# Kernel optimization log

Hardware: AMD Instinct MI355X
Metric: run time of the kernel (lower is better)

Reference implementation:

```python
import jax, jax.numpy as jnp
import numpy as np

N = 2048      # num_nodes
B = 16        # batch
D_IN = 2      # input_dim per node
UNITS = 64    # rnn_units
F = D_IN + UNITS   # concat feature size = 66
M = 3         # num_matrices = (1 support + 1 adp hop)*K(=1) + 1 identity
E = N * 16    # sparse support edges (avg degree 16)


def _spmm(rows, cols, vals, x):
    # sparse support @ x, x: (N, K); equivalent of torch.sparse.mm
    return jax.ops.segment_sum(vals[:, None] * x[cols], rows, num_segments=N)


def _gconv(inputs, state, W, support_rows, support_cols, support_vals, adp):
    # inputs: (B, N*D_IN), state: (B, N*units) -> out: (B, N*out_dim)
    x = jnp.concatenate([inputs.reshape(B, N, -1), state.reshape(B, N, -1)], axis=2)  # (B,N,F)
    f = x.shape[2]
    x0 = x.transpose(1, 2, 0).reshape(N, f * B)                # (N, F*B)
    # diffusion step 1 over the single random_walk support
    x1 = _spmm(support_rows, support_cols, support_vals, x0)   # (N, F*B)
    # adaptive adjacency, k_hop=1 -> adp_lst = [adp], applied to x0
    x_temp = x0.reshape(N, f, B).transpose(2, 0, 1)            # (B,N,F)
    x2 = jnp.einsum('bnm,bmf->bnf', adp, x_temp)               # (B,N,F)
    x2 = x2.transpose(1, 2, 0).reshape(N, f * B)
    xs = jnp.stack([x0, x1, x2], axis=0)                       # (M,N,F*B)
    xs = xs.reshape(M, N, f, B).transpose(3, 1, 2, 0).reshape(B * N, f * M)
    out = xs @ W                                               # (B*N, out_dim)  (no bias: source never adds it)
    return out.reshape(B, N * W.shape[1])


def setup_inputs() -> dict:
    key = jax.random.key(0)
    ks = jax.random.split(key, 8)
    inputs = jax.random.normal(ks[0], (B, N * D_IN), dtype=jnp.float32)
    hx = jax.random.normal(ks[1], (B, N * UNITS), dtype=jnp.float32)
    adp = jax.random.uniform(ks[2], (B, N, N), dtype=jnp.float32) / N  # ~row-stochastic adaptive adj
    support_rows = jax.random.randint(ks[3], (E,), 0, N, dtype=jnp.int32)
    support_cols = jax.random.randint(ks[4], (E,), 0, N, dtype=jnp.int32)
    support_vals = jax.random.uniform(ks[5], (E,), dtype=jnp.float32) / 16.0
    W_ru = jax.random.normal(ks[6], (F * M, 2 * UNITS), dtype=jnp.float32) * 0.05
    W_c = jax.random.normal(ks[7], (F * M, UNITS), dtype=jnp.float32) * 0.05
    return dict(inputs=inputs, hx=hx, adp=adp, support_rows=support_rows,
                support_cols=support_cols, support_vals=support_vals,
                W_ru=W_ru, W_c=W_c, time_axis=0)


def reference(inputs, hx, adp, support_rows, support_cols, support_vals, W_ru, W_c, time_axis):
    # GRU with graph convolution gates (use_gc_for_ru=True, activation=tanh)
    ru = jax.nn.sigmoid(_gconv(inputs, hx, W_ru, support_rows, support_cols, support_vals, adp))
    ru = ru.reshape(B, N, 2 * UNITS)
    r = ru[..., :UNITS].reshape(B, N * UNITS)
    u = ru[..., UNITS:].reshape(B, N * UNITS)
    c = jnp.tanh(_gconv(inputs, r * hx, W_c, support_rows, support_cols, support_vals, adp))
    return u * hx + (1.0 - u) * c
```

## Files before the change

### kernel.cpp

```cpp
#include <hip/hip_runtime.h>
#include <cstdint>
#include <cstddef>

#define DN 2048
#define DB 16
#define DE 32768
#define FPAD 96

typedef __bf16 bf16x8 __attribute__((ext_vector_type(8)));
typedef float f32x4 __attribute__((ext_vector_type(4)));

__global__ __launch_bounds__(256) void prep_kernel(
    const float* __restrict__ inputs, const float* __restrict__ hx,
    const float* __restrict__ Wru, const float* __restrict__ Wc,
    __bf16* __restrict__ xcat1, __bf16* __restrict__ xcat2,
    __bf16* __restrict__ wtru, __bf16* __restrict__ wtc,
    int* __restrict__ cnt) {
  int idx = blockIdx.x * 256 + threadIdx.x;
  const int T1 = DB * DN * FPAD;
  if (idx < 2 * T1) {
    int which = idx >= T1 ? 1 : 0;
    int i = idx - which * T1;
    int f = i % FPAD;
    int bn = i / FPAD;
    int n = bn & (DN - 1);
    int b = bn >> 11;
    __bf16 v = (__bf16)0.0f;
    if (f < 2) v = (__bf16)inputs[(b << 12) + n * 2 + f];
    else if (f < 66 && !which) v = (__bf16)hx[((size_t)b << 17) + (n << 6) + (f - 2)];
    if (which) xcat2[i] = v; else xcat1[i] = v;
  } else {
    int j = idx - 2 * T1;
    if (j < 384 * FPAD) {
      int k = j % FPAD, o = j / FPAD;
      wtru[j] = (k < 66) ? (__bf16)Wru[(k * 3 + (o >> 7)) * 128 + (o & 127)] : (__bf16)0.0f;
    } else {
      j -= 384 * FPAD;
      if (j < 192 * FPAD) {
        int k = j % FPAD, o = j / FPAD;
        wtc[j] = (k < 66) ? (__bf16)Wc[(k * 3 + (o >> 6)) * 64 + (o & 63)] : (__bf16)0.0f;
      } else {
        j -= 192 * FPAD;
        if (j < DN) cnt[j] = 0;
      }
    }
  }
}

__global__ __launch_bounds__(512) void csr_count(const int* __restrict__ rows,
                                                 int* __restrict__ cnt) {
  int e = blockIdx.x * 512 + threadIdx.x;
  atomicAdd(&cnt[rows[e]], 1);
}

__global__ __launch_bounds__(1024) void csr_scan(const int* __restrict__ cnt,
                                                 int* __restrict__ csr_ptr,
                                                 int* __restrict__ off) {
  __shared__ int sa[DN];
  __shared__ int sb[DN];
  int t = threadIdx.x;
  int c0 = cnt[t], c1 = cnt[t + 1024];
  sa[t] = c0; sa[t + 1024] = c1;
  __syncthreads();
  int* src = sa; int* dst = sb;
  for (int o = 1; o < DN; o <<= 1) {
    for (int i = t; i < DN; i += 1024) {
      int v = src[i];
      if (i >= o) v += src[i - o];
      dst[i] = v;
    }
    __syncthreads();
    int* tmp = src; src = dst; dst = tmp;
  }
  int e0 = src[t] - c0;
  int e1 = src[t + 1024] - c1;
  csr_ptr[t] = e0; csr_ptr[t + 1024] = e1;
  off[t] = e0; off[t + 1024] = e1;
  if (t == 0) csr_ptr[DN] = DE;
}

__global__ __launch_bounds__(512) void csr_scatter(
    const int* __restrict__ rows, const int* __restrict__ cols,
    const float* __restrict__ vals, int* __restrict__ off,
    int* __restrict__ csr_col, float* __restrict__ csr_val) {
  int e = blockIdx.x * 512 + threadIdx.x;
  int r = rows[e];
  int p = atomicAdd(&off[r], 1);
  csr_col[p] = cols[e];
  csr_val[p] = vals[e];
}

template <int OD>
__global__ __launch_bounds__(256) void small_gemm(
    const __bf16* __restrict__ A, const __bf16* __restrict__ Bt,
    float* __restrict__ Y0, __bf16* __restrict__ y1b, __bf16* __restrict__ y2b) {
  __shared__ __attribute__((aligned(16))) __bf16 As[128 * 104];
  __shared__ __attribute__((aligned(16))) __bf16 Bs[64 * 104];
  int tid = threadIdx.x;
  int wave = tid >> 6, lane = tid & 63;
  int lrow = lane & 15, quad = lane >> 4;
  int r0 = blockIdx.x * 128;
  int c0 = blockIdx.y * 64;
  const uint4* gA = (const uint4*)(A + (size_t)r0 * FPAD);
  const uint4* gB = (const uint4*)(Bt + (size_t)c0 * FPAD);
  uint4* sA = (uint4*)As;
  uint4* sB = (uint4*)Bs;
#pragma unroll
  for (int i = 0; i < 6; ++i) {
    int s = i * 256 + tid;
    int r = s / 12, c4 = s % 12;
    sA[r * 13 + c4] = gA[r * 12 + c4];
  }
#pragma unroll
  for (int i = 0; i < 3; ++i) {
    int s = i * 256 + tid;
    int r = s / 12, c4 = s % 12;
    sB[r * 13 + c4] = gB[r * 12 + c4];
  }
  __syncthreads();
  int wm = wave >> 1, wn = wave & 1;
  f32x4 acc[4][2];
#pragma unroll
  for (int mt = 0; mt < 4; ++mt)
#pragma unroll
    for (int nt = 0; nt < 2; ++nt) acc[mt][nt] = (f32x4){0.f, 0.f, 0.f, 0.f};
#pragma unroll
  for (int kk = 0; kk < 3; ++kk) {
    bf16x8 af[4], bv[2];
#pragma unroll
    for (int mt = 0; mt < 4; ++mt)
      af[mt] = *(const bf16x8*)(As + (wm * 64 + mt * 16 + lrow) * 104 + kk * 32 + quad * 8);
#pragma unroll
    for (int nt = 0; nt < 2; ++nt)
      bv[nt] = *(const bf16x8*)(Bs + (wn * 32 + nt * 16 + lrow) * 104 + kk * 32 + quad * 8);
#pragma unroll
    for (int mt = 0; mt < 4; ++mt)
#pragma unroll
      for (int nt = 0; nt < 2; ++nt)
        acc[mt][nt] = __builtin_amdgcn_mfma_f32_16x16x32_bf16(af[mt], bv[nt], acc[mt][nt], 0, 0, 0);
  }
#pragma unroll
  for (int mt = 0; mt < 4; ++mt)
#pragma unroll
    for (int nt = 0; nt < 2; ++nt)
#pragma unroll
      for (int r = 0; r < 4; ++r) {
        int row = r0 + wm * 64 + mt * 16 + quad * 4 + r;
        int col = c0 + wn * 32 + nt * 16 + lrow;
        float v = acc[mt][nt][r];
        int g = col >> ((OD == 128) ? 7 : 6);
        int oo = col & (OD - 1);
        size_t oi = (size_t)row * OD + oo;
        if (g == 0) Y0[oi] = v;
        else if (g == 1) y1b[oi] = (__bf16)v;
        else y2b[oi] = (__bf16)v;
      }
}

template <int OD>
__global__ __launch_bounds__(256) void gather_pre(
    float* __restrict__ Y0, const __bf16* __restrict__ y1b,
    const int* __restrict__ csr_ptr, const int* __restrict__ csr_col,
    const float* __restrict__ csr_val) {
  constexpr int SH = (OD == 128) ? 7 : 6;
  int idx = blockIdx.x * 256 + threadIdx.x;
  int o = idx & (OD - 1);
  int bn = idx >> SH;
  int n = bn & (DN - 1);
  int b = bn >> 11;
  float acc = Y0[idx];
  int e1 = csr_ptr[n + 1];
  const __bf16* yb = y1b + ((size_t)b << 11) * OD;
  for (int e = csr_ptr[n]; e < e1; ++e)
    acc += csr_val[e] * (float)yb[(size_t)csr_col[e] * OD + o];
  Y0[idx] = acc;
}

template <int OD>
__global__ void transpose_y2(const __bf16* __restrict__ y2b, __bf16* __restrict__ y2t) {
  __shared__ __bf16 tile[32][33];
  int b = blockIdx.z;
  int mb = blockIdx.x * 32, ob = blockIdx.y * 32;
  int tx = threadIdx.x, ty = threadIdx.y;
#pragma unroll
  for (int i = 0; i < 4; ++i)
    tile[ty + i * 8][tx] = y2b[(size_t)(b * DN + mb + ty + i * 8) * OD + ob + tx];
  __syncthreads();
#pragma unroll
  for (int i = 0; i < 4; ++i)
    y2t[(size_t)(b * OD + ob + ty + i * 8) * DN + mb + tx] = tile[tx][ty + i * 8];
}

template <int OD, bool IS_RU>
__global__ __launch_bounds__(256, 4) void adp_gemm(
    const float* __restrict__ adp, const __bf16* __restrict__ y2t,
    const float* __restrict__ pre, const float* __restrict__ hx,
    float* __restrict__ u_buf, __bf16* __restrict__ xcat2,
    float* __restrict__ outp) {
  constexpr int NT = OD / 32;
  int tid = threadIdx.x;
  int wave = tid >> 6, lane = tid & 63;
  int lrow = lane & 15, quad = lane >> 4;
  int hw = blockIdx.x;
  int swz = (hw & 7) * 128 + (hw >> 3);
  int b = swz >> 6;
  int row0 = (swz & 63) * 32;
  int wm = wave >> 1, wn = wave & 1;
  int arow = row0 + wm * 16 + lrow;
  const float* Ap = adp + ((size_t)b * DN + arow) * DN + quad * 8;
  const __bf16* Bb = y2t + (size_t)b * OD * (size_t)DN + quad * 8;
  const __bf16* Bp[NT];
#pragma unroll
  for (int nt = 0; nt < NT; ++nt)
    Bp[nt] = Bb + (size_t)(wn * (NT * 16) + nt * 16 + lrow) * DN;

  f32x4 acc[NT];
#pragma unroll
  for (int nt = 0; nt < NT; ++nt) acc[nt] = (f32x4){0.f, 0.f, 0.f, 0.f};

  f32x4 aE0, aE1, aE2, aE3, aO0, aO1, aO2, aO3;
#define LOADA(c, a0, a1, a2, a3)                 \
  {                                              \
    const float* p_ = Ap + (size_t)(c) * 64;     \
    a0 = *(const f32x4*)p_;                      \
    a1 = *(const f32x4*)(p_ + 4);                \
    a2 = *(const f32x4*)(p_ + 32);               \
    a3 = *(const f32x4*)(p_ + 36);               \
  }

  LOADA(0, aE0, aE1, aE2, aE3);
  LOADA(1, aO0, aO1, aO2, aO3);

#pragma unroll 1
  for (int c = 0; c < DN / 64; c += 2) {
    {
      bf16x8 bv[2][NT];
#pragma unroll
      for (int kk = 0; kk < 2; ++kk)
#pragma unroll
        for (int nt = 0; nt < NT; ++nt)
          bv[kk][nt] = *(const bf16x8*)(Bp[nt] + c * 64 + kk * 32);
      bf16x8 af0, af1;
#pragma unroll
      for (int j = 0; j < 4; ++j) {
        af0[j] = (__bf16)aE0[j]; af0[4 + j] = (__bf16)aE1[j];
        af1[j] = (__bf16)aE2[j]; af1[4 + j] = (__bf16)aE3[j];
      }
      if (c + 2 < DN / 64) LOADA(c + 2, aE0, aE1, aE2, aE3);
#pragma unroll
      for (int nt = 0; nt < NT; ++nt)
        acc[nt] = __builtin_amdgcn_mfma_f32_16x16x32_bf16(af0, bv[0][nt], acc[nt], 0, 0, 0);
#pragma unroll
      for (int nt = 0; nt < NT; ++nt)
        acc[nt] = __builtin_amdgcn_mfma_f32_16x16x32_bf16(af1, bv[1][nt], acc[nt], 0, 0, 0);
    }
    {
      bf16x8 bv[2][NT];
#pragma unroll
      for (int kk = 0; kk < 2; ++kk)
#pragma unroll
        for (int nt = 0; nt < NT; ++nt)
          bv[kk][nt] = *(const bf16x8*)(Bp[nt] + (c + 1) * 64 + kk * 32);
      bf16x8 af0, af1;
#pragma unroll
      for (int j = 0; j < 4; ++j) {
        af0[j] = (__bf16)aO0[j]; af0[4 + j] = (__bf16)aO1[j];
        af1[j] = (__bf16)aO2[j]; af1[4 + j] = (__bf16)aO3[j];
      }
      if (c + 3 < DN / 64) LOADA(c + 3, aO0, aO1, aO2, aO3);
#pragma unroll
      for (int nt = 0; nt < NT; ++nt)
        acc[nt] = __builtin_amdgcn_mfma_f32_16x16x32_bf16(af0, bv[0][nt], acc[nt], 0, 0, 0);
#pragma unroll
      for (int nt = 0; nt < NT; ++nt)
        acc[nt] = __builtin_amdgcn_mfma_f32_16x16x32_bf16(af1, bv[1][nt], acc[nt], 0, 0, 0);
    }
  }
#undef LOADA

#pragma unroll
  for (int nt = 0; nt < NT; ++nt)
#pragma unroll
    for (int r = 0; r < 4; ++r) {
      int n = row0 + wm * 16 + quad * 4 + r;
      int o = wn * (NT * 16) + nt * 16 + lrow;
      float g = acc[nt][r] + pre[((size_t)b * DN + n) * OD + o];
      if (IS_RU) {
        float s = 1.f / (1.f + __expf(-g));
        if (o < 64) {
          float hxv = hx[((size_t)b << 17) + n * 64 + o];
          xcat2[((size_t)b * DN + n) * FPAD + 2 + o] = (__bf16)(s * hxv);
        } else {
          u_buf[((size_t)b * DN + n) * 64 + (o - 64)] = s;
        }
      } else {
        float cval = 1.f - 2.f / (__expf(2.f * g) + 1.f);
        float u = u_buf[((size_t)b * DN + n) * 64 + o];
        float hxv = hx[((size_t)b << 17) + n * 64 + o];
        outp[((size_t)b << 17) + n * 64 + o] = u * hxv + (1.f - u) * cval;
      }
    }
}

extern "C" void kernel_launch(void* const* d_in, const int* in_sizes, int n_in,
                              void* d_out, int out_size, void* d_ws, size_t ws_size,
                              hipStream_t stream) {
  const float* inputs = (const float*)d_in[0];
  const float* hx     = (const float*)d_in[1];
  const float* adp    = (const float*)d_in[2];
  const int* srows    = (const int*)d_in[3];
  const int* scols    = (const int*)d_in[4];
  const float* svals  = (const float*)d_in[5];
  const float* Wru    = (const float*)d_in[6];
  const float* Wc     = (const float*)d_in[7];
  float* outp = (float*)d_out;

  char* w = (char*)d_ws;
  auto carve = [&](size_t bytes) -> char* {
    char* p = w;
    w += (bytes + 255) & ~(size_t)255;
    return p;
  };
  int*    csr_ptr = (int*)   carve((DN + 1) * sizeof(int));
  int*    csr_col = (int*)   carve(DE * sizeof(int));
  float*  csr_val = (float*) carve(DE * sizeof(float));
  int*    cnt     = (int*)   carve(DN * sizeof(int));
  int*    off     = (int*)   carve(DN * sizeof(int));
  __bf16* xcat1   = (__bf16*)carve((size_t)DB * DN * FPAD * 2);
  __bf16* xcat2   = (__bf16*)carve((size_t)DB * DN * FPAD * 2);
  __bf16* wtru    = (__bf16*)carve(384 * FPAD * 2);
  __bf16* wtc     = (__bf16*)carve(192 * FPAD * 2);
  float*  Y0      = (float*) carve((size_t)DB * DN * 128 * 4);
  __bf16* y1b     = (__bf16*)carve((size_t)DB * DN * 128 * 2);
  __bf16* y2b     = (__bf16*)carve((size_t)DB * DN * 128 * 2);
  __bf16* y2t     = (__bf16*)carve((size_t)DB * DN * 128 * 2);
  float*  u_buf   = (float*) carve((size_t)DB * DN * 64 * 4);
  (void)ws_size; (void)in_sizes; (void)n_in; (void)out_size;

  prep_kernel<<<24800, 256, 0, stream>>>(inputs, hx, Wru, Wc, xcat1, xcat2,
                                         wtru, wtc, cnt);
  csr_count<<<64, 512, 0, stream>>>(srows, cnt);
  csr_scan<<<1, 1024, 0, stream>>>(cnt, csr_ptr, off);
  csr_scatter<<<64, 512, 0, stream>>>(srows, scols, svals, off, csr_col, csr_val);

  small_gemm<128><<<dim3(256, 6), 256, 0, stream>>>(xcat1, wtru, Y0, y1b, y2b);
  gather_pre<128><<<16384, 256, 0, stream>>>(Y0, y1b, csr_ptr, csr_col, csr_val);
  transpose_y2<128><<<dim3(64, 4, 16), dim3(32, 8), 0, stream>>>(y2b, y2t);
  adp_gemm<128, true><<<1024, 256, 0, stream>>>(
      adp, y2t, Y0, hx, u_buf, xcat2, outp);

  small_gemm<64><<<dim3(256, 3), 256, 0, stream>>>(xcat2, wtc, Y0, y1b, y2b);
  gather_pre<64><<<8192, 256, 0, stream>>>(Y0, y1b, csr_ptr, csr_col, csr_val);
  transpose_y2<64><<<dim3(64, 2, 16), dim3(32, 8), 0, stream>>>(y2b, y2t);
  adp_gemm<64, false><<<1024, 256, 0, stream>>>(
      adp, y2t, Y0, hx, u_buf, xcat2, outp);
}
```

Baseline: 796.1 us.

## Write y2 in MFMA-fragment packed layout and drop transpose kernels

The small GEMM now writes the adp-path projection directly into a packed layout that matches the B-fragment order of the adp GEMM MFMA, so the separate transpose kernels are removed. The adp GEMM is retiled to 16-row blocks with each wave owning a column slice. It also uses twice as many blocks and a higher occupancy hint, and drops the manual double-buffered A prefetch. This removes two launches and a round trip through memory and makes B loads fully coalesced. The cost is that each adp row tile is now read by fewer columns per block, and the A stream loses its explicit software prefetch.

```diff
diff --git a/kernel.cpp b/kernel.cpp
--- a/kernel.cpp
+++ b/kernel.cpp
@@ -8,6 +8,7 @@
 #define FPAD 96
 
 typedef __bf16 bf16x8 __attribute__((ext_vector_type(8)));
+typedef __bf16 bf16x4 __attribute__((ext_vector_type(4)));
 typedef float f32x4 __attribute__((ext_vector_type(4)));
 
 __global__ __launch_bounds__(256) void prep_kernel(
@@ -93,7 +94,7 @@
 template <int OD>
 __global__ __launch_bounds__(256) void small_gemm(
     const __bf16* __restrict__ A, const __bf16* __restrict__ Bt,
-    float* __restrict__ Y0, __bf16* __restrict__ y1b, __bf16* __restrict__ y2b) {
+    float* __restrict__ Y0, __bf16* __restrict__ y1b, __bf16* __restrict__ y2p) {
   __shared__ __attribute__((aligned(16))) __bf16 As[128 * 104];
   __shared__ __attribute__((aligned(16))) __bf16 Bs[64 * 104];
   int tid = threadIdx.x;
@@ -142,19 +143,31 @@
 #pragma unroll
   for (int mt = 0; mt < 4; ++mt)
 #pragma unroll
-    for (int nt = 0; nt < 2; ++nt)
-#pragma unroll
-      for (int r = 0; r < 4; ++r) {
-        int row = r0 + wm * 64 + mt * 16 + quad * 4 + r;
-        int col = c0 + wn * 32 + nt * 16 + lrow;
-        float v = acc[mt][nt][r];
-        int g = col >> ((OD == 128) ? 7 : 6);
-        int oo = col & (OD - 1);
-        size_t oi = (size_t)row * OD + oo;
-        if (g == 0) Y0[oi] = v;
-        else if (g == 1) y1b[oi] = (__bf16)v;
-        else y2b[oi] = (__bf16)v;
+    for (int nt = 0; nt < 2; ++nt) {
+      int col = c0 + wn * 32 + nt * 16 + lrow;
+      int g = col >> ((OD == 128) ? 7 : 6);
+      int oo = col & (OD - 1);
+      int rowb = r0 + wm * 64 + mt * 16 + quad * 4;
+      if (g == 2) {
+        int bb = rowb >> 11;
+        int n_ = rowb & 2047;
+        bf16x4 v;
+#pragma unroll
+        for (int r = 0; r < 4; ++r) v[r] = (__bf16)acc[mt][nt][r];
+        size_t off = ((((size_t)bb * (OD / 16) + (oo >> 4)) * 64 + (n_ >> 5)) * 4 +
+                      ((n_ >> 3) & 3)) * 128 + (oo & 15) * 8 + (n_ & 7);
+        *(bf16x4*)(y2p + off) = v;
+      } else {
+#pragma unroll
+        for (int r = 0; r < 4; ++r) {
+          int row = rowb + r;
+          float v = acc[mt][nt][r];
+          size_t oi = (size_t)row * OD + oo;
+          if (g == 0) Y0[oi] = v;
+          else y1b[oi] = (__bf16)v;
+        }
       }
+    }
 }
 
 template <int OD>
@@ -176,114 +189,65 @@
   Y0[idx] = acc;
 }
 
-template <int OD>
-__global__ void transpose_y2(const __bf16* __restrict__ y2b, __bf16* __restrict__ y2t) {
-  __shared__ __bf16 tile[32][33];
-  int b = blockIdx.z;
-  int mb = blockIdx.x * 32, ob = blockIdx.y * 32;
-  int tx = threadIdx.x, ty = threadIdx.y;
-#pragma unroll
-  for (int i = 0; i < 4; ++i)
-    tile[ty + i * 8][tx] = y2b[(size_t)(b * DN + mb + ty + i * 8) * OD + ob + tx];
-  __syncthreads();
-#pragma unroll
-  for (int i = 0; i < 4; ++i)
-    y2t[(size_t)(b * OD + ob + ty + i * 8) * DN + mb + tx] = tile[tx][ty + i * 8];
-}
-
 template <int OD, bool IS_RU>
-__global__ __launch_bounds__(256, 4) void adp_gemm(
-    const float* __restrict__ adp, const __bf16* __restrict__ y2t,
+__global__ __launch_bounds__(256, 6) void adp_gemm(
+    const float* __restrict__ adp, const __bf16* __restrict__ y2p,
     const float* __restrict__ pre, const float* __restrict__ hx,
     float* __restrict__ u_buf, __bf16* __restrict__ xcat2,
     float* __restrict__ outp) {
-  constexpr int NT = OD / 32;
+  constexpr int NT = OD / 64;
   int tid = threadIdx.x;
   int wave = tid >> 6, lane = tid & 63;
   int lrow = lane & 15, quad = lane >> 4;
   int hw = blockIdx.x;
-  int swz = (hw & 7) * 128 + (hw >> 3);
-  int b = swz >> 6;
-  int row0 = (swz & 63) * 32;
-  int wm = wave >> 1, wn = wave & 1;
-  int arow = row0 + wm * 16 + lrow;
-  const float* Ap = adp + ((size_t)b * DN + arow) * DN + quad * 8;
-  const __bf16* Bb = y2t + (size_t)b * OD * (size_t)DN + quad * 8;
-  const __bf16* Bp[NT];
+  int swz = (hw & 7) * 256 + (hw >> 3);
+  int b = swz >> 7;
+  int row0 = (swz & 127) * 16;
+  const float* Ap = adp + ((size_t)b * DN + row0 + lrow) * DN + quad * 8;
+  const __bf16* Bq[NT];
+#pragma unroll
+  for (int nt = 0; nt < NT; ++nt) {
+    int ob = wave * NT + nt;
+    Bq[nt] = y2p + ((size_t)b * (OD / 16) + ob) * (64 * 512) + lane * 8;
+  }
+
+  f32x4 acc[NT];
+#pragma unroll
+  for (int nt = 0; nt < NT; ++nt) acc[nt] = (f32x4){0.f, 0.f, 0.f, 0.f};
+
+#pragma unroll 1
+  for (int c = 0; c < DN / 64; ++c) {
+    bf16x8 bv[2][NT];
+#pragma unroll
+    for (int kk = 0; kk < 2; ++kk)
+#pragma unroll
+      for (int nt = 0; nt < NT; ++nt)
+        bv[kk][nt] = *(const bf16x8*)(Bq[nt] + c * 1024 + kk * 512);
+    const float* p_ = Ap + (size_t)c * 64;
+    f32x4 a00 = *(const f32x4*)p_;
+    f32x4 a01 = *(const f32x4*)(p_ + 4);
+    f32x4 a10 = *(const f32x4*)(p_ + 32);
+    f32x4 a11 = *(const f32x4*)(p_ + 36);
+    bf16x8 af0, af1;
+#pragma unroll
+    for (int j = 0; j < 4; ++j) {
+      af0[j] = (__bf16)a00[j]; af0[4 + j] = (__bf16)a01[j];
+      af1[j] = (__bf16)a10[j]; af1[4 + j] = (__bf16)a11[j];
+    }
+#pragma unroll
+    for (int nt = 0; nt < NT; ++nt)
+      acc[nt] = __builtin_amdgcn_mfma_f32_16x16x32_bf16(af0, bv[0][nt], acc[nt], 0, 0, 0);
+#pragma unroll
+    for (int nt = 0; nt < NT; ++nt)
+      acc[nt] = __builtin_amdgcn_mfma_f32_16x16x32_bf16(af1, bv[1][nt], acc[nt], 0, 0, 0);
+  }
+
 #pragma unroll
   for (int nt = 0; nt < NT; ++nt)
-    Bp[nt] = Bb + (size_t)(wn * (NT * 16) + nt * 16 + lrow) * DN;
-
-  f32x4 acc[NT];
-#pragma unroll
-  for (int nt = 0; nt < NT; ++nt) acc[nt] = (f32x4){0.f, 0.f, 0.f, 0.f};
-
-  f32x4 aE0, aE1, aE2, aE3, aO0, aO1, aO2, aO3;
-#define LOADA(c, a0, a1, a2, a3)                 \
-  {                                              \
-    const float* p_ = Ap + (size_t)(c) * 64;     \
-    a0 = *(const f32x4*)p_;                      \
-    a1 = *(const f32x4*)(p_ + 4);                \
-    a2 = *(const f32x4*)(p_ + 32);               \
-    a3 = *(const f32x4*)(p_ + 36);               \
-  }
-
-  LOADA(0, aE0, aE1, aE2, aE3);
-  LOADA(1, aO0, aO1, aO2, aO3);
-
-#pragma unroll 1
-  for (int c = 0; c < DN / 64; c += 2) {
-    {
-      bf16x8 bv[2][NT];
-#pragma unroll
-      for (int kk = 0; kk < 2; ++kk)
-#pragma unroll
-        for (int nt = 0; nt < NT; ++nt)
-          bv[kk][nt] = *(const bf16x8*)(Bp[nt] + c * 64 + kk * 32);
-      bf16x8 af0, af1;
-#pragma unroll
-      for (int j = 0; j < 4; ++j) {
-        af0[j] = (__bf16)aE0[j]; af0[4 + j] = (__bf16)aE1[j];
-        af1[j] = (__bf16)aE2[j]; af1[4 + j] = (__bf16)aE3[j];
-      }
-      if (c + 2 < DN / 64) LOADA(c + 2, aE0, aE1, aE2, aE3);
-#pragma unroll
-      for (int nt = 0; nt < NT; ++nt)
-        acc[nt] = __builtin_amdgcn_mfma_f32_16x16x32_bf16(af0, bv[0][nt], acc[nt], 0, 0, 0);
-#pragma unroll
-      for (int nt = 0; nt < NT; ++nt)
-        acc[nt] = __builtin_amdgcn_mfma_f32_16x16x32_bf16(af1, bv[1][nt], acc[nt], 0, 0, 0);
-    }
-    {
-      bf16x8 bv[2][NT];
-#pragma unroll
-      for (int kk = 0; kk < 2; ++kk)
-#pragma unroll
-        for (int nt = 0; nt < NT; ++nt)
-          bv[kk][nt] = *(const bf16x8*)(Bp[nt] + (c + 1) * 64 + kk * 32);
-      bf16x8 af0, af1;
-#pragma unroll
-      for (int j = 0; j < 4; ++j) {
-        af0[j] = (__bf16)aO0[j]; af0[4 + j] = (__bf16)aO1[j];
-        af1[j] = (__bf16)aO2[j]; af1[4 + j] = (__bf16)aO3[j];
-      }
-      if (c + 3 < DN / 64) LOADA(c + 3, aO0, aO1, aO2, aO3);
-#pragma unroll
-      for (int nt = 0; nt < NT; ++nt)
-        acc[nt] = __builtin_amdgcn_mfma_f32_16x16x32_bf16(af0, bv[0][nt], acc[nt], 0, 0, 0);
-#pragma unroll
-      for (int nt = 0; nt < NT; ++nt)
-        acc[nt] = __builtin_amdgcn_mfma_f32_16x16x32_bf16(af1, bv[1][nt], acc[nt], 0, 0, 0);
-    }
-  }
-#undef LOADA
-
-#pragma unroll
-  for (int nt = 0; nt < NT; ++nt)
 #pragma unroll
     for (int r = 0; r < 4; ++r) {
-      int n = row0 + wm * 16 + quad * 4 + r;
-      int o = wn * (NT * 16) + nt * 16 + lrow;
+      int n = row0 + quad * 4 + r;
+      int o = wave * (NT * 16) + nt * 16 + lrow;
       float g = acc[nt][r] + pre[((size_t)b * DN + n) * OD + o];
       if (IS_RU) {
         float s = 1.f / (1.f + __expf(-g));
@@ -333,9 +297,9 @@
   float*  Y0      = (float*) carve((size_t)DB * DN * 128 * 4);
   __bf16* y1b     = (__bf16*)carve((size_t)DB * DN * 128 * 2);
   __bf16* y2b     = (__bf16*)carve((size_t)DB * DN * 128 * 2);
-  __bf16* y2t     = (__bf16*)carve((size_t)DB * DN * 128 * 2);
+  __bf16* y2p     = (__bf16*)carve((size_t)DB * DN * 128 * 2);
   float*  u_buf   = (float*) carve((size_t)DB * DN * 64 * 4);
-  (void)ws_size; (void)in_sizes; (void)n_in; (void)out_size;
+  (void)ws_size; (void)in_sizes; (void)n_in; (void)out_size; (void)y2b;
 
   prep_kernel<<<24800, 256, 0, stream>>>(inputs, hx, Wru, Wc, xcat1, xcat2,
                                          wtru, wtc, cnt);
@@ -343,15 +307,13 @@
   csr_scan<<<1, 1024, 0, stream>>>(cnt, csr_ptr, off);
   csr_scatter<<<64, 512, 0, stream>>>(srows, scols, svals, off, csr_col, csr_val);
 
-  small_gemm<128><<<dim3(256, 6), 256, 0, stream>>>(xcat1, wtru, Y0, y1b, y2b);
+  small_gemm<128><<<dim3(256, 6), 256, 0, stream>>>(xcat1, wtru, Y0, y1b, y2p);
   gather_pre<128><<<16384, 256, 0, stream>>>(Y0, y1b, csr_ptr, csr_col, csr_val);
-  transpose_y2<128><<<dim3(64, 4, 16), dim3(32, 8), 0, stream>>>(y2b, y2t);
-  adp_gemm<128, true><<<1024, 256, 0, stream>>>(
-      adp, y2t, Y0, hx, u_buf, xcat2, outp);
-
-  small_gemm<64><<<dim3(256, 3), 256, 0, stream>>>(xcat2, wtc, Y0, y1b, y2b);
+  adp_gemm<128, true><<<2048, 256, 0, stream>>>(
+      adp, y2p, Y0, hx, u_buf, xcat2, outp);
+
+  small_gemm<64><<<dim3(256, 3), 256, 0, stream>>>(xcat2, wtc, Y0, y1b, y2p);
   gather_pre<64><<<8192, 256, 0, stream>>>(Y0, y1b, csr_ptr, csr_col, csr_val);
-  transpose_y2<64><<<dim3(64, 2, 16), dim3(32, 8), 0, stream>>>(y2b, y2t);
-  adp_gemm<64, false><<<1024, 256, 0, stream>>>(
-      adp, y2t, Y0, hx, u_buf, xcat2, outp);
-}
+  adp_gemm<64, false><<<2048, 256, 0, stream>>>(
+      adp, y2p, Y0, hx, u_buf, xcat2, outp);
+}
```

New measurement: 801.1 us. About the same (+0.6%).
